# Kernel optimization log

Measured on AMD Instinct MI355X. Metric: run time of the kernel, lower is better.

## Reference

```python
import jax, jax.numpy as jnp
import numpy as np

T = 8192        # tokens (batch*seq)
D = 1024        # d_model
H = 4096        # expert hidden = 4*d_model
E = 16          # num_expert
K = 2           # moe_top_k


def setup_inputs() -> dict:
    key = jax.random.key(0)
    ks = jax.random.split(key, 7)
    s_in = 1.0 / np.sqrt(D)
    s_h = 1.0 / np.sqrt(H)
    return {
        "moe_inp": jax.random.normal(ks[0], (T, D), dtype=jnp.float32),
        "Wg": jax.random.normal(ks[1], (D, E), dtype=jnp.float32) * s_in,
        "bg": jnp.zeros((E,), dtype=jnp.float32),
        "W1": jax.random.normal(ks[2], (E, D, H), dtype=jnp.float32) * s_in,
        "b1": jnp.zeros((E, H), dtype=jnp.float32),
        "W2": jax.random.normal(ks[3], (E, H, D), dtype=jnp.float32) * s_h,
        "b2": jnp.zeros((E, D), dtype=jnp.float32),
    }


def reference(moe_inp, Wg, bg, W1, b1, W2, b2):
    # --- NaiveGate: linear -> top-k -> softmax over selected logits ---
    logits = moe_inp @ Wg + bg                      # [T, E]
    topk_val, topk_idx = jax.lax.top_k(logits, K)   # [T, K]
    gate_score = jax.nn.softmax(topk_val, axis=-1)  # [T, K]

    # Per-(token, expert) combine weight: sum of gate scores of slots routed to e.
    # Equivalent to scatter(dispatch) -> expert MLP -> gather(combine) weighted sum.
    onehot = jax.nn.one_hot(topk_idx, E, dtype=moe_inp.dtype)  # [T, K, E]
    comb_w = jnp.einsum('tk,tke->te', gate_score, onehot)      # [T, E]

    out = jnp.zeros_like(moe_inp)
    for e in range(E):  # fixed small expert count
        h = jax.nn.relu(moe_inp @ W1[e] + b1[e])   # [T, H]
        y = h @ W2[e] + b2[e]                      # [T, D]
        out = out + comb_w[:, e:e + 1] * y
    return out
```

## Files before the change

kernel.cpp:

```cpp
#include <hip/hip_runtime.h>
#include <hip/hip_bf16.h>
#include <stdint.h>


#define Tn 8192
#define Dn 1024
#define Hn 4096
#define En 16

typedef __attribute__((ext_vector_type(8))) short bf16x8;
typedef __attribute__((ext_vector_type(4))) float f32x4;

__device__ __forceinline__ unsigned short f2bf(float f) {
    union { __hip_bfloat16 h; unsigned short u; } cv;
    cv.h = __float2bfloat16(f);
    return cv.u;
}
__device__ __forceinline__ float bf2f(unsigned short u) {
    union { unsigned int i; float f; } cv;
    cv.i = ((unsigned int)u) << 16;
    return cv.f;
}

__device__ __forceinline__ void gload_lds16(const void* gptr, void* lptr) {
    __builtin_amdgcn_global_load_lds(
        (const __attribute__((address_space(1))) uint32_t*)gptr,
        (__attribute__((address_space(3))) uint32_t*)lptr, 16, 0, 0);
}

__device__ __forceinline__ int swz_tile(int v, int total) {
    int q = total >> 3, r = total & 7;
    int x = v & 7, k = v >> 3;
    int b = (x < r) ? x * (q + 1) : r * (q + 1) + (x - r) * q;
    return b + k;
}

__device__ __forceinline__ int find_e(const int* __restrict__ mb, int gm) {
    int e = 0;
#pragma unroll
    for (int i = 1; i < En; i++) e += (mb[i] <= gm) ? 1 : 0;
    return e;
}

__device__ __forceinline__ void waitvm4()  { asm volatile("s_waitcnt vmcnt(4)" ::: "memory"); }
__device__ __forceinline__ void waitvm0()  { asm volatile("s_waitcnt vmcnt(0)" ::: "memory"); }
__device__ __forceinline__ void barrier_raw() { asm volatile("s_barrier" ::: "memory"); }

__device__ __forceinline__ bool better(float va, int ia, float vb, int ib) {
    return (va > vb) || (va == vb && ia < ib);
}

__global__ __launch_bounds__(256) void gate_kernel(
    const float* __restrict__ x, const float* __restrict__ Wg,
    const float* __restrict__ bg,
    int* cnt, int* tok_e, int* tok_pos, float* tok_w)
{
    __shared__ float wgt[16 * 1028];
    int tid = threadIdx.x;
    int t0 = blockIdx.x * 16;

#pragma unroll
    for (int i = 0; i < 64; i++) {
        int idx = i * 256 + tid;
        int k = idx >> 4, e = idx & 15;
        wgt[e * 1028 + k] = Wg[idx];
    }
    __syncthreads();

    int tok = tid >> 4, e = tid & 15;
    const float4* xr = reinterpret_cast<const float4*>(x + (size_t)(t0 + tok) * Dn);
    const float4* wr = reinterpret_cast<const float4*>(&wgt[e * 1028]);
    float acc = 0.f;
#pragma unroll 8
    for (int q = 0; q < 256; q++) {
        float4 xv = xr[q], wv = wr[q];
        acc += xv.x * wv.x + xv.y * wv.y + xv.z * wv.z + xv.w * wv.w;
    }
    acc += bg[e];

    float v0 = acc, v1 = -1e30f;
    int i0 = e, i1 = -1;
#pragma unroll
    for (int m = 1; m < 16; m <<= 1) {
        float ov0 = __shfl_xor(v0, m, 16); int oi0 = __shfl_xor(i0, m, 16);
        float ov1 = __shfl_xor(v1, m, 16); int oi1 = __shfl_xor(i1, m, 16);
        if (better(ov0, oi0, v0, i0)) {
            if (better(v0, i0, ov1, oi1)) { v1 = v0; i1 = i0; }
            else                          { v1 = ov1; i1 = oi1; }
            v0 = ov0; i0 = oi0;
        } else if (better(ov0, oi0, v1, i1)) {
            v1 = ov0; i1 = oi0;
        }
    }
    if (e == 0) {
        float ex = __expf(v1 - v0);
        float w0 = 1.f / (1.f + ex);
        float w1 = ex / (1.f + ex);
        int p0 = atomicAdd(&cnt[i0], 1);
        int p1 = atomicAdd(&cnt[i1], 1);
        int t = t0 + tok;
        tok_e[t * 2 + 0] = i0; tok_e[t * 2 + 1] = i1;
        tok_pos[t * 2 + 0] = p0; tok_pos[t * 2 + 1] = p1;
        tok_w[t * 2 + 0] = w0; tok_w[t * 2 + 1] = w1;
    }
}

__global__ void scan_kernel(const int* cnt, int* base, int* mb)
{
    if (threadIdx.x == 0 && blockIdx.x == 0) {
        int b = 0, m = 0;
        for (int e = 0; e < En; e++) {
            base[e] = b; mb[e] = m;
            b += cnt[e];
            m += (cnt[e] + 127) >> 7;
        }
        base[En] = b; mb[En] = m;
    }
}

__global__ __launch_bounds__(256) void gather_kernel(
    const float* __restrict__ x, const int* tok_e, const int* tok_pos,
    const int* base, unsigned short* xg)
{
    int t = blockIdx.x; int tid = threadIdx.x;
    int e0 = tok_e[2 * t], e1 = tok_e[2 * t + 1];
    int r0 = base[e0] + tok_pos[2 * t];
    int r1 = base[e1] + tok_pos[2 * t + 1];
    float4 v = *reinterpret_cast<const float4*>(x + (size_t)t * Dn + tid * 4);
    ushort4 u;
    u.x = f2bf(v.x); u.y = f2bf(v.y); u.z = f2bf(v.z); u.w = f2bf(v.w);
    *reinterpret_cast<ushort4*>(xg + (size_t)r0 * Dn + tid * 4) = u;
    *reinterpret_cast<ushort4*>(xg + (size_t)r1 * Dn + tid * 4) = u;
}

__global__ __launch_bounds__(512) void convT_kernel(
    const float* __restrict__ src, unsigned short* __restrict__ dst, int R, int C)
{
    int e = blockIdx.z;
    const float* s = src + (size_t)e * R * C;
    unsigned short* d = dst + (size_t)e * R * C;
    __shared__ float tile[64][65];
    int r0 = blockIdx.y * 64, c0 = blockIdx.x * 64;
    int tr = threadIdx.x >> 4;
    int tc4 = (threadIdx.x & 15) * 4;
    float4 v0 = *reinterpret_cast<const float4*>(s + (size_t)(r0 + tr) * C + c0 + tc4);
    float4 v1 = *reinterpret_cast<const float4*>(s + (size_t)(r0 + tr + 32) * C + c0 + tc4);
    tile[tr][tc4 + 0] = v0.x; tile[tr][tc4 + 1] = v0.y;
    tile[tr][tc4 + 2] = v0.z; tile[tr][tc4 + 3] = v0.w;
    tile[tr + 32][tc4 + 0] = v1.x; tile[tr + 32][tc4 + 1] = v1.y;
    tile[tr + 32][tc4 + 2] = v1.z; tile[tr + 32][tc4 + 3] = v1.w;
    __syncthreads();
    ushort4 u0, u1;
    u0.x = f2bf(tile[tc4 + 0][tr]);      u1.x = f2bf(tile[tc4 + 0][tr + 32]);
    u0.y = f2bf(tile[tc4 + 1][tr]);      u1.y = f2bf(tile[tc4 + 1][tr + 32]);
    u0.z = f2bf(tile[tc4 + 2][tr]);      u1.z = f2bf(tile[tc4 + 2][tr + 32]);
    u0.w = f2bf(tile[tc4 + 3][tr]);      u1.w = f2bf(tile[tc4 + 3][tr + 32]);
    *reinterpret_cast<ushort4*>(d + (size_t)(c0 + tr) * R + r0 + tc4) = u0;
    *reinterpret_cast<ushort4*>(d + (size_t)(c0 + tr + 32) * R + r0 + tc4) = u1;
}

template<bool G1>
__global__ __launch_bounds__(256, 4) void gemm128_kernel(
    const unsigned short* __restrict__ Ag, const unsigned short* __restrict__ Bg,
    const float* __restrict__ bias, unsigned short* __restrict__ outb,
    const int* __restrict__ cnt, const int* __restrict__ base,
    const int* __restrict__ mb)
{
    constexpr int KDIM = G1 ? Dn : Hn;
    constexpr int NOUT = G1 ? Hn : Dn;
    constexpr int NTN = NOUT / 128;
    constexpr int NT = KDIM / 32;
    __shared__ unsigned short ldsA[2][64 * 64];
    __shared__ unsigned short ldsB[2][64 * 64];

    int totalgm = mb[En];
    int total = totalgm * NTN;

    int tid = threadIdx.x;
    int lane = tid & 63;
    int w = tid >> 6;
    int wm = (w >> 1) * 64, wn = (w & 1) * 64;
    int lr16 = lane & 15, lk = lane >> 4;
    int lj = lk * 4;

    int lrow0 = tid >> 3;
    int lrow1 = (tid + 256) >> 3;
    int ch0 = (tid & 7) ^ (lrow0 & 7);
    int ch1 = (tid & 7) ^ (lrow1 & 7);
    int grow0 = lrow0 * 2 + (ch0 >> 2), kc0 = ch0 & 3;
    int grow1 = lrow1 * 2 + (ch1 >> 2), kc1 = ch1 & 3;

    int aoff[4], boff[4];
#pragma unroll
    for (int m = 0; m < 4; m++) {
        int row = wm + m * 16 + lr16;
        int lr = row >> 1;
        aoff[m] = lr * 64 + (((((row & 1) << 2) | lk) ^ (lr & 7)) << 3);
    }
#pragma unroll
    for (int n = 0; n < 4; n++) {
        int row = wn + n * 16 + lr16;
        int lr = row >> 1;
        boff[n] = lr * 64 + (((((row & 1) << 2) | lk) ^ (lr & 7)) << 3);
    }

    for (int v = blockIdx.x; v < total; v += gridDim.x) {
        int tile = swz_tile(v, total);
        int gm = tile / NTN;
        int nt = tile % NTN;
        int e = find_e(mb, gm);
        int mtile = gm - mb[e];
        int M_e = cnt[e];
        int m0 = mtile * 128, n0 = nt * 128;
        int rowbase0 = base[e] + m0;
        const unsigned short* Ab = Ag + (size_t)rowbase0 * KDIM;
        const unsigned short* Bb = Bg + ((size_t)e * NOUT + n0) * KDIM;

        const unsigned short* aS0 = Ab + (size_t)grow0 * KDIM + kc0 * 8;
        const unsigned short* aS1 = Ab + (size_t)grow1 * KDIM + kc1 * 8;
        const unsigned short* bS0 = Bb + (size_t)grow0 * KDIM + kc0 * 8;
        const unsigned short* bS1 = Bb + (size_t)grow1 * KDIM + kc1 * 8;

        f32x4 acc[4][4];
#pragma unroll
        for (int m = 0; m < 4; m++)
#pragma unroll
            for (int n = 0; n < 4; n++) acc[m][n] = (f32x4){0.f, 0.f, 0.f, 0.f};

        auto stage = [&](int t) {
            char* sa = (char*)ldsA[t & 1];
            char* sb = (char*)ldsB[t & 1];
            int k0 = t * 32;
            gload_lds16(aS0 + k0, sa + tid * 16);
            gload_lds16(aS1 + k0, sa + (tid + 256) * 16);
            gload_lds16(bS0 + k0, sb + tid * 16);
            gload_lds16(bS1 + k0, sb + (tid + 256) * 16);
        };

        stage(0);
        stage(1);

        for (int t = 0; t < NT; ++t) {
            if (t + 1 < NT) waitvm4();
            else            waitvm0();
            barrier_raw();
            const unsigned short* sa = ldsA[t & 1];
            const unsigned short* sb = ldsB[t & 1];
            bf16x8 a[4], b[4];
#pragma unroll
            for (int n = 0; n < 4; n++) b[n] = *(const bf16x8*)(sb + boff[n]);
#pragma unroll
            for (int m = 0; m < 4; m++) a[m] = *(const bf16x8*)(sa + aoff[m]);
            __builtin_amdgcn_s_setprio(1);
#pragma unroll
            for (int m = 0; m < 4; m++)
#pragma unroll
                for (int n = 0; n < 4; n++)
                    acc[m][n] = __builtin_amdgcn_mfma_f32_16x16x32_bf16(b[n], a[m], acc[m][n], 0, 0, 0);
            __builtin_amdgcn_s_setprio(0);
            barrier_raw();
            if (t + 2 < NT) stage(t + 2);
        }

        const float* be = bias + (size_t)e * NOUT;
#pragma unroll
        for (int m = 0; m < 4; m++) {
            int rt = wm + m * 16 + lr16;
            if (m0 + rt < M_e) {
                size_t rowoff = (size_t)(rowbase0 + rt) * NOUT;
#pragma unroll
                for (int n = 0; n < 4; n++) {
                    int col0e = n0 + wn + n * 16 + lj;
                    float4 bs = *reinterpret_cast<const float4*>(be + col0e);
                    float v0 = acc[m][n][0] + bs.x;
                    float v1 = acc[m][n][1] + bs.y;
                    float v2 = acc[m][n][2] + bs.z;
                    float v3 = acc[m][n][3] + bs.w;
                    ushort4 u;
                    if constexpr (G1) {
                        u.x = f2bf(fmaxf(v0, 0.f));
                        u.y = f2bf(fmaxf(v1, 0.f));
                        u.z = f2bf(fmaxf(v2, 0.f));
                        u.w = f2bf(fmaxf(v3, 0.f));
                    } else {
                        u.x = f2bf(v0); u.y = f2bf(v1);
                        u.z = f2bf(v2); u.w = f2bf(v3);
                    }
                    *reinterpret_cast<ushort4*>(outb + rowoff + col0e) = u;
                }
            }
        }
    }
}

__global__ __launch_bounds__(256) void combine_kernel(
    const unsigned short* __restrict__ y,
    const int* __restrict__ tok_e, const int* __restrict__ tok_pos,
    const int* __restrict__ base, const float* __restrict__ tok_w,
    float* __restrict__ out)
{
    int t = blockIdx.x, tid = threadIdx.x;
    int e0 = tok_e[2 * t], e1 = tok_e[2 * t + 1];
    int r0 = base[e0] + tok_pos[2 * t];
    int r1 = base[e1] + tok_pos[2 * t + 1];
    float w0 = tok_w[2 * t], w1 = tok_w[2 * t + 1];
    ushort4 a = *reinterpret_cast<const ushort4*>(y + (size_t)r0 * Dn + tid * 4);
    ushort4 b = *reinterpret_cast<const ushort4*>(y + (size_t)r1 * Dn + tid * 4);
    float4 o;
    o.x = w0 * bf2f(a.x) + w1 * bf2f(b.x);
    o.y = w0 * bf2f(a.y) + w1 * bf2f(b.y);
    o.z = w0 * bf2f(a.z) + w1 * bf2f(b.z);
    o.w = w0 * bf2f(a.w) + w1 * bf2f(b.w);
    *reinterpret_cast<float4*>(out + (size_t)t * Dn + tid * 4) = o;
}

extern "C" void kernel_launch(void* const* d_in, const int* in_sizes, int n_in,
                              void* d_out, int out_size, void* d_ws, size_t ws_size,
                              hipStream_t stream)
{
    const float* x  = (const float*)d_in[0];
    const float* Wg = (const float*)d_in[1];
    const float* bg = (const float*)d_in[2];
    const float* W1 = (const float*)d_in[3];
    const float* b1 = (const float*)d_in[4];
    const float* W2 = (const float*)d_in[5];
    const float* b2 = (const float*)d_in[6];
    float* out = (float*)d_out;

    char* ws = (char*)d_ws;
    size_t off = 0;
    auto alloc = [&](size_t bytes) {
        size_t o = off; off += (bytes + 255) & ~(size_t)255; return o;
    };
    const int ROWS = Tn * 2;
    const int RCAP = ROWS + 256;

    unsigned short* Wt = (unsigned short*)(ws + alloc((size_t)En * Hn * Dn * 2));
    unsigned short* xg = (unsigned short*)(ws + alloc((size_t)RCAP * Dn * 2));
    unsigned short* hg = (unsigned short*)(ws + alloc((size_t)RCAP * Hn * 2));
    unsigned short* yv = (unsigned short*)(ws + alloc((size_t)RCAP * Dn * 2));
    int*   cnt     = (int*)(ws + alloc(En * 4));
    int*   base    = (int*)(ws + alloc((En + 1) * 4));
    int*   mb      = (int*)(ws + alloc((En + 1) * 4));
    int*   tok_e   = (int*)(ws + alloc(Tn * 2 * 4));
    int*   tok_pos = (int*)(ws + alloc(Tn * 2 * 4));
    float* tok_w   = (float*)(ws + alloc(Tn * 2 * 4));
    (void)ws_size; (void)in_sizes; (void)n_in; (void)out_size;

    hipMemsetAsync(cnt, 0, En * 4, stream);

    gate_kernel<<<Tn / 16, 256, 0, stream>>>(x, Wg, bg, cnt, tok_e, tok_pos, tok_w);
    scan_kernel<<<1, 64, 0, stream>>>(cnt, base, mb);
    gather_kernel<<<Tn, 256, 0, stream>>>(x, tok_e, tok_pos, base, xg);

    convT_kernel<<<dim3(Hn / 64, Dn / 64, En), 512, 0, stream>>>(W1, Wt, Dn, Hn);
    gemm128_kernel<true><<<1024, 256, 0, stream>>>(
        xg, Wt, b1, hg, cnt, base, mb);

    convT_kernel<<<dim3(Dn / 64, Hn / 64, En), 512, 0, stream>>>(W2, Wt, Hn, Dn);
    gemm128_kernel<false><<<1024, 256, 0, stream>>>(
        hg, Wt, b2, yv, cnt, base, mb);

    combine_kernel<<<Tn, 256, 0, stream>>>(yv, tok_e, tok_pos, base, tok_w, out);
}
```

Measured before the change: 712.1 us.

## Split-K second GEMM into two halves and group tiles for L2 reuse

```diff
diff --git a/kernel.cpp b/kernel.cpp
--- a/kernel.cpp
+++ b/kernel.cpp
@@ -163,18 +163,21 @@
 __global__ __launch_bounds__(256, 4) void gemm128_kernel(
     const unsigned short* __restrict__ Ag, const unsigned short* __restrict__ Bg,
     const float* __restrict__ bias, unsigned short* __restrict__ outb,
+    size_t ystride,
     const int* __restrict__ cnt, const int* __restrict__ base,
     const int* __restrict__ mb)
 {
     constexpr int KDIM = G1 ? Dn : Hn;
+    constexpr int KLEN = G1 ? Dn : (Hn / 2);
     constexpr int NOUT = G1 ? Hn : Dn;
-    constexpr int NTN = NOUT / 128;
-    constexpr int NT = KDIM / 32;
+    constexpr int NT = KLEN / 32;
     __shared__ unsigned short ldsA[2][64 * 64];
     __shared__ unsigned short ldsB[2][64 * 64];
 
     int totalgm = mb[En];
-    int total = totalgm * NTN;
+    int ptotal;
+    if constexpr (G1) ptotal = (((totalgm + 7) >> 3) << 8);
+    else              ptotal = (((totalgm + 3) >> 2) << 6);
 
     int tid = threadIdx.x;
     int lane = tid & 63;
@@ -204,17 +207,32 @@
         boff[n] = lr * 64 + (((((row & 1) << 2) | lk) ^ (lr & 7)) << 3);
     }
 
-    for (int v = blockIdx.x; v < total; v += gridDim.x) {
-        int tile = swz_tile(v, total);
-        int gm = tile / NTN;
-        int nt = tile % NTN;
+    for (int v = blockIdx.x; v < ptotal; v += gridDim.x) {
+        int tile = swz_tile(v, ptotal);
+        int gm, nt, kh;
+        if constexpr (G1) {
+            int group = tile >> 6, within = tile & 63;
+            int gmb = group >> 2, ntb = group & 3;
+            gm = (gmb << 3) + (within >> 3);
+            nt = (ntb << 3) + (within & 7);
+            kh = 0;
+        } else {
+            int group = tile >> 4, within = tile & 15;
+            int gmb = group >> 2, knb = group & 3;
+            gm = (gmb << 2) + (within >> 2);
+            int knt = (knb << 2) + (within & 3);
+            kh = knt >> 3; nt = knt & 7;
+        }
+        if (gm >= totalgm) continue;
+
         int e = find_e(mb, gm);
         int mtile = gm - mb[e];
         int M_e = cnt[e];
         int m0 = mtile * 128, n0 = nt * 128;
+        int kbase = kh * KLEN;
         int rowbase0 = base[e] + m0;
-        const unsigned short* Ab = Ag + (size_t)rowbase0 * KDIM;
-        const unsigned short* Bb = Bg + ((size_t)e * NOUT + n0) * KDIM;
+        const unsigned short* Ab = Ag + (size_t)rowbase0 * KDIM + kbase;
+        const unsigned short* Bb = Bg + ((size_t)e * NOUT + n0) * KDIM + kbase;
 
         const unsigned short* aS0 = Ab + (size_t)grow0 * KDIM + kc0 * 8;
         const unsigned short* aS1 = Ab + (size_t)grow1 * KDIM + kc1 * 8;
@@ -262,7 +280,9 @@
             if (t + 2 < NT) stage(t + 2);
         }
 
+        bool addb = G1 || (kh == 0);
         const float* be = bias + (size_t)e * NOUT;
+        unsigned short* ob = outb + (G1 ? 0 : (size_t)kh * ystride);
 #pragma unroll
         for (int m = 0; m < 4; m++) {
             int rt = wm + m * 16 + lr16;
@@ -271,7 +291,8 @@
 #pragma unroll
                 for (int n = 0; n < 4; n++) {
                     int col0e = n0 + wn + n * 16 + lj;
-                    float4 bs = *reinterpret_cast<const float4*>(be + col0e);
+                    float4 bs = addb ? *reinterpret_cast<const float4*>(be + col0e)
+                                     : (float4){0.f, 0.f, 0.f, 0.f};
                     float v0 = acc[m][n][0] + bs.x;
                     float v1 = acc[m][n][1] + bs.y;
                     float v2 = acc[m][n][2] + bs.z;
@@ -286,7 +307,7 @@
                         u.x = f2bf(v0); u.y = f2bf(v1);
                         u.z = f2bf(v2); u.w = f2bf(v3);
                     }
-                    *reinterpret_cast<ushort4*>(outb + rowoff + col0e) = u;
+                    *reinterpret_cast<ushort4*>(ob + rowoff + col0e) = u;
                 }
             }
         }
@@ -294,7 +315,7 @@
 }
 
 __global__ __launch_bounds__(256) void combine_kernel(
-    const unsigned short* __restrict__ y,
+    const unsigned short* __restrict__ y, size_t ystride,
     const int* __restrict__ tok_e, const int* __restrict__ tok_pos,
     const int* __restrict__ base, const float* __restrict__ tok_w,
     float* __restrict__ out)
@@ -304,13 +325,16 @@
     int r0 = base[e0] + tok_pos[2 * t];
     int r1 = base[e1] + tok_pos[2 * t + 1];
     float w0 = tok_w[2 * t], w1 = tok_w[2 * t + 1];
-    ushort4 a = *reinterpret_cast<const ushort4*>(y + (size_t)r0 * Dn + tid * 4);
-    ushort4 b = *reinterpret_cast<const ushort4*>(y + (size_t)r1 * Dn + tid * 4);
+    const unsigned short* y1 = y + ystride;
+    ushort4 a0 = *reinterpret_cast<const ushort4*>(y  + (size_t)r0 * Dn + tid * 4);
+    ushort4 a1 = *reinterpret_cast<const ushort4*>(y1 + (size_t)r0 * Dn + tid * 4);
+    ushort4 b0 = *reinterpret_cast<const ushort4*>(y  + (size_t)r1 * Dn + tid * 4);
+    ushort4 b1 = *reinterpret_cast<const ushort4*>(y1 + (size_t)r1 * Dn + tid * 4);
     float4 o;
-    o.x = w0 * bf2f(a.x) + w1 * bf2f(b.x);
-    o.y = w0 * bf2f(a.y) + w1 * bf2f(b.y);
-    o.z = w0 * bf2f(a.z) + w1 * bf2f(b.z);
-    o.w = w0 * bf2f(a.w) + w1 * bf2f(b.w);
+    o.x = w0 * (bf2f(a0.x) + bf2f(a1.x)) + w1 * (bf2f(b0.x) + bf2f(b1.x));
+    o.y = w0 * (bf2f(a0.y) + bf2f(a1.y)) + w1 * (bf2f(b0.y) + bf2f(b1.y));
+    o.z = w0 * (bf2f(a0.z) + bf2f(a1.z)) + w1 * (bf2f(b0.z) + bf2f(b1.z));
+    o.w = w0 * (bf2f(a0.w) + bf2f(a1.w)) + w1 * (bf2f(b0.w) + bf2f(b1.w));
     *reinterpret_cast<float4*>(out + (size_t)t * Dn + tid * 4) = o;
 }
 
@@ -334,11 +358,12 @@
     };
     const int ROWS = Tn * 2;
     const int RCAP = ROWS + 256;
+    const size_t YSTR = (size_t)RCAP * Dn;
 
     unsigned short* Wt = (unsigned short*)(ws + alloc((size_t)En * Hn * Dn * 2));
     unsigned short* xg = (unsigned short*)(ws + alloc((size_t)RCAP * Dn * 2));
     unsigned short* hg = (unsigned short*)(ws + alloc((size_t)RCAP * Hn * 2));
-    unsigned short* yv = (unsigned short*)(ws + alloc((size_t)RCAP * Dn * 2));
+    unsigned short* yv = (unsigned short*)(ws + alloc(2 * YSTR * 2));
     int*   cnt     = (int*)(ws + alloc(En * 4));
     int*   base    = (int*)(ws + alloc((En + 1) * 4));
     int*   mb      = (int*)(ws + alloc((En + 1) * 4));
@@ -355,11 +380,11 @@
 
     convT_kernel<<<dim3(Hn / 64, Dn / 64, En), 512, 0, stream>>>(W1, Wt, Dn, Hn);
     gemm128_kernel<true><<<1024, 256, 0, stream>>>(
-        xg, Wt, b1, hg, cnt, base, mb);
+        xg, Wt, b1, hg, 0, cnt, base, mb);
 
     convT_kernel<<<dim3(Dn / 64, Hn / 64, En), 512, 0, stream>>>(W2, Wt, Hn, Dn);
     gemm128_kernel<false><<<1024, 256, 0, stream>>>(
-        hg, Wt, b2, yv, cnt, base, mb);
-
-    combine_kernel<<<Tn, 256, 0, stream>>>(yv, tok_e, tok_pos, base, tok_w, out);
-}
+        hg, Wt, b2, yv, YSTR, cnt, base, mb);
+
+    combine_kernel<<<Tn, 256, 0, stream>>>(yv, YSTR, tok_e, tok_pos, base, tok_w, out);
+}
```

Measured after the change: 695.2 us (median of 2 runs). 1.02x faster.
